# Kernel optimization log

Measured on AMD Instinct MI355X. Metric: run time of the kernel, lower is better.

## Reference

```python
import jax, jax.numpy as jnp
import numpy as np

N_HEADS = 16
LOCAL_WINDOW = 512
ROPE_BASE = 10000.0


def _rotate_half(x):
    # interleaved rotate: out[..., 2i] = -x[..., 2i+1], out[..., 2i+1] = x[..., 2i]
    x1 = x[..., 0::2]
    x2 = x[..., 1::2]
    return jnp.stack((-x2, x1), axis=-1).reshape(x.shape)


def _rope_cache(T, hd, dtype):
    half = hd // 2
    inv_freq = 1.0 / (ROPE_BASE ** (jnp.arange(half, dtype=dtype) / half))
    t = jnp.arange(T, dtype=dtype)
    freqs = t[:, None] * inv_freq[None, :]  # [T, half]
    cos = jnp.repeat(jnp.cos(freqs), 2, axis=-1)  # [T, hd]
    sin = jnp.repeat(jnp.sin(freqs), 2, axis=-1)
    return cos, sin


def setup_inputs() -> dict:
    key = jax.random.key(0)
    k1, k2, k3, k4 = jax.random.split(key, 4)
    B, T, C = 2, 2048, 1024
    x = jax.random.normal(k1, (B, T, C), dtype=jnp.float32)
    Wqkv = jax.random.normal(k2, (3 * C, C), dtype=jnp.float32) * 0.02
    Wproj = jax.random.normal(k3, (C, C), dtype=jnp.float32) * 0.02
    bproj = jax.random.normal(k4, (C,), dtype=jnp.float32) * 0.02
    return {"x": x, "Wqkv": Wqkv, "Wproj": Wproj, "bproj": bproj}


def reference(x, Wqkv, Wproj, bproj):
    B, T, C = x.shape
    H = N_HEADS
    hd = C // H
    qkv = (x @ Wqkv.T).reshape(B, T, 3, H, hd).transpose(2, 0, 3, 1, 4)  # [3,B,H,T,hd]
    q, k, v = qkv[0], qkv[1], qkv[2]
    cos, sin = _rope_cache(T, hd, x.dtype)
    cos = cos[None, None]  # [1,1,T,hd]
    sin = sin[None, None]
    q = q * cos + _rotate_half(q) * sin
    k = k * cos + _rotate_half(k) * sin
    scale = 1.0 / jnp.sqrt(jnp.asarray(hd, dtype=x.dtype))
    scores = jnp.einsum('bhqd,bhkd->bhqk', q, k) * scale  # [B,H,T,T]
    i = jnp.arange(T)[:, None]
    j = jnp.arange(T)[None, :]
    allow = (j <= i) & (jnp.abs(i - j) <= LOCAL_WINDOW)  # causal & local band
    scores = jnp.where(allow[None, None], scores, jnp.asarray(-jnp.inf, dtype=x.dtype))
    attn = jax.nn.softmax(scores, axis=-1)
    y = jnp.einsum('bhqk,bhkd->bhqd', attn, v)  # [B,H,T,hd]
    y = y.transpose(0, 2, 1, 3).reshape(B, T, C)
    return y @ Wproj.T + bproj
```

## Files before the change

### kernel.cpp

```cpp
#include <hip/hip_runtime.h>
#include <math.h>

#define B_   2
#define T_   2048
#define C_   1024
#define H_   16
#define HD_  64
#define WIN_ 512
#define BT_  (B_ * T_)

typedef __bf16 bf16x8 __attribute__((ext_vector_type(8)));
typedef float  f32x4  __attribute__((ext_vector_type(4)));
typedef unsigned int u32x2 __attribute__((ext_vector_type(2)));

__device__ __forceinline__ f32x4 mfma16(bf16x8 a, bf16x8 b, f32x4 c) {
    return __builtin_amdgcn_mfma_f32_16x16x32_bf16(a, b, c, 0, 0, 0);
}
__device__ __forceinline__ unsigned short f2b(float f) {
    __bf16 h = (__bf16)f;
    unsigned short u;
    __builtin_memcpy(&u, &h, 2);
    return u;
}
__device__ __forceinline__ void async_copy16(__bf16* lds, const __bf16* g) {
    __builtin_amdgcn_global_load_lds(
        (const __attribute__((address_space(1))) void*)g,
        (__attribute__((address_space(3))) void*)lds,
        16, 0, 0);
}

#define TR16(dst, va, OFFLIT) \
    asm volatile("ds_read_b64_tr_b16 %0, %1 offset:" OFFLIT : "=v"(dst) : "v"(va))

__device__ __forceinline__ bf16x8 combine_tr(u32x2 a, u32x2 b) {
    union { unsigned u[4]; bf16x8 v; } x;
    x.u[0] = a[0]; x.u[1] = a[1]; x.u[2] = b[0]; x.u[3] = b[1];
    return x.v;
}

__global__ void rope_table_k(float* __restrict__ cosT, float* __restrict__ sinT) {
    int gid = blockIdx.x * blockDim.x + threadIdx.x;
    if (gid >= T_ * 32) return;
    int t = gid >> 5, j = gid & 31;
    float inv = powf(10000.0f, -(float)j / 32.0f);
    float f = (float)t * inv;
    cosT[gid] = cosf(f);
    sinT[gid] = sinf(f);
}

__global__ void cvt_bf16_k(const float* __restrict__ src, __bf16* __restrict__ dst, int n8) {
    int gid = blockIdx.x * blockDim.x + threadIdx.x;
    if (gid >= n8) return;
    float4 a = *(const float4*)&src[(size_t)gid * 8];
    float4 b = *(const float4*)&src[(size_t)gid * 8 + 4];
    bf16x8 o;
    o[0] = (__bf16)a.x; o[1] = (__bf16)a.y; o[2] = (__bf16)a.z; o[3] = (__bf16)a.w;
    o[4] = (__bf16)b.x; o[5] = (__bf16)b.y; o[6] = (__bf16)b.z; o[7] = (__bf16)b.w;
    *(bf16x8*)&dst[(size_t)gid * 8] = o;
}

template<bool OUT_BF16, bool ROPE>
__global__ __launch_bounds__(256) void gemm_bt_mfma(
        const __bf16* __restrict__ A, const __bf16* __restrict__ Bm,
        const float* __restrict__ bias, void* __restrict__ Cv,
        int M, int N, int K,
        const float* __restrict__ cosT, const float* __restrict__ sinT)
{
    __shared__ __bf16 As[128 * 32];
    __shared__ __bf16 Bs[128 * 32];
    const int tid  = threadIdx.x;
    const int w    = tid >> 6;
    const int lane = tid & 63;
    const int c    = lane & 15;
    const int g    = lane >> 4;
    const int bm0  = blockIdx.y * 128;
    const int bn0  = blockIdx.x * 128;
    const int wm0  = (w >> 1) * 64;
    const int wn0  = (w & 1) * 64;

    f32x4 acc[4][4] = {};

    for (int k0 = 0; k0 < K; k0 += 32) {
        #pragma unroll
        for (int it = 0; it < 2; ++it) {
            int slot = it * 256 + tid;
            int r    = slot >> 2;
            int c8   = (slot & 3) * 8;
            async_copy16(&As[slot * 8], &A[(size_t)(bm0 + r) * K + k0 + c8]);
            async_copy16(&Bs[slot * 8], &Bm[(size_t)(bn0 + r) * K + k0 + c8]);
        }
        __syncthreads();
        bf16x8 af[4], bfr[4];
        #pragma unroll
        for (int m = 0; m < 4; ++m)
            af[m] = *(const bf16x8*)&As[(wm0 + m * 16 + c) * 32 + g * 8];
        #pragma unroll
        for (int n = 0; n < 4; ++n)
            bfr[n] = *(const bf16x8*)&Bs[(wn0 + n * 16 + c) * 32 + g * 8];
        #pragma unroll
        for (int m = 0; m < 4; ++m)
            #pragma unroll
            for (int n = 0; n < 4; ++n)
                acc[m][n] = mfma16(af[m], bfr[n], acc[m][n]);
        __syncthreads();
    }

    if (ROPE) {
        #pragma unroll
        for (int m = 0; m < 4; ++m) {
            #pragma unroll
            for (int r2 = 0; r2 < 4; ++r2) {
                const int row = bm0 + wm0 + m * 16 + g * 4 + r2;
                const int t = row & (T_ - 1);
                #pragma unroll
                for (int n = 0; n < 4; ++n) {
                    const int cbase = bn0 + wn0 + n * 16;
                    const int cc = cbase + c;
                    float v = acc[m][n][r2];
                    float outv;
                    if (cbase < 2048) {
                        float prt = __shfl_xor(v, 1);
                        int jj = (cc & 63) >> 1;
                        float cs = cosT[t * 32 + jj];
                        float sn = sinT[t * 32 + jj];
                        outv = (cc & 1) ? (v * cs + prt * sn) : (v * cs - prt * sn);
                    } else {
                        outv = v;
                    }
                    ((__bf16*)Cv)[(size_t)row * N + cc] = (__bf16)outv;
                }
            }
        }
    } else {
        #pragma unroll
        for (int m = 0; m < 4; ++m) {
            int rr = bm0 + wm0 + m * 16 + g * 4;
            #pragma unroll
            for (int n = 0; n < 4; ++n) {
                int cc = bn0 + wn0 + n * 16 + c;
                float bv = (!OUT_BF16 && bias) ? bias[cc] : 0.f;
                #pragma unroll
                for (int r2 = 0; r2 < 4; ++r2) {
                    float v = acc[m][n][r2] + bv;
                    if (OUT_BF16) ((__bf16*)Cv)[(size_t)(rr + r2) * N + cc] = (__bf16)v;
                    else          ((float*)Cv)[(size_t)(rr + r2) * N + cc] = v;
                }
            }
        }
    }
}

__global__ __launch_bounds__(256) void attn_k(const __bf16* __restrict__ qkv,
                                              __bf16* __restrict__ y)
{
    __shared__ __align__(16) unsigned short Ks[64 * 72];
    __shared__ __align__(16) unsigned short Ps[64 * 72];
    __shared__ __align__(16) unsigned short Vs[4 * 1040];

    const int tid  = threadIdx.x;
    const int lane = tid & 63;
    const int w    = tid >> 6;
    const int c    = lane & 15;
    const int g    = lane >> 4;

    const int q0 = blockIdx.x * 64;
    const int h  = blockIdx.y;
    const int b  = blockIdx.z;

    bf16x8 qa[2];
    {
        const int qrow = q0 + w * 16 + c;
        const __bf16* qp = qkv + (size_t)(b * T_ + qrow) * 3072 + h * 64 + g * 8;
        bf16x8 r0 = *(const bf16x8*)qp;
        bf16x8 r1 = *(const bf16x8*)(qp + 32);
        #pragma unroll
        for (int e = 0; e < 8; ++e) {
            qa[0][e] = (__bf16)((float)r0[e] * 0.125f);
            qa[1][e] = (__bf16)((float)r1[e] * 0.125f);
        }
    }

    float m_run[4] = {-1e30f, -1e30f, -1e30f, -1e30f};
    float l_run[4] = {0.f, 0.f, 0.f, 0.f};
    f32x4 o[4] = {};

    unsigned vs_lane;
    {
        auto* p3 = (__attribute__((address_space(3))) const unsigned short*)Vs;
        vs_lane = (unsigned)(unsigned long long)p3 + (unsigned)(g * 256 + c * 8);
    }

    const int j_start = (q0 >= WIN_) ? (q0 - WIN_) : 0;

    for (int j0 = j_start; j0 <= q0; j0 += 64) {
        __syncthreads();
        #pragma unroll
        for (int it = 0; it < 4; ++it) {
            int slot = tid + it * 256;
            int row  = slot >> 4;
            int d4   = (slot & 15) << 2;
            const __bf16* kp = qkv + (size_t)(b * T_ + j0 + row) * 3072 + 1024 + h * 64 + d4;
            *(ushort4*)&Ks[row * 72 + d4] = *(const ushort4*)kp;
            *(ushort4*)&Vs[(d4 >> 4) * 1040 + row * 16 + (d4 & 15)] = *(const ushort4*)(kp + 1024);
        }
        __syncthreads();

        f32x4 sc[4];
        #pragma unroll
        for (int nt = 0; nt < 4; ++nt) {
            const bf16x8 b0 = *(const bf16x8*)&Ks[(nt * 16 + c) * 72 + g * 8];
            const bf16x8 b1 = *(const bf16x8*)&Ks[(nt * 16 + c) * 72 + 32 + g * 8];
            f32x4 s = {0.f, 0.f, 0.f, 0.f};
            s = mfma16(qa[0], b0, s);
            s = mfma16(qa[1], b1, s);
            sc[nt] = s;
        }

        const int rlo = q0 + w * 16;
        const bool need_mask = (j0 + 63 > rlo) || (rlo + 15 - j0 > WIN_);
        if (need_mask) {
            #pragma unroll
            for (int reg = 0; reg < 4; ++reg) {
                const int i_abs = rlo + g * 4 + reg;
                #pragma unroll
                for (int nt = 0; nt < 4; ++nt) {
                    int j_abs = j0 + nt * 16 + c;
                    bool ok = (j_abs <= i_abs) && (i_abs - j_abs <= WIN_);
                    sc[nt][reg] = ok ? sc[nt][reg] : -1e30f;
                }
            }
        }

        float pmax[4];
        #pragma unroll
        for (int reg = 0; reg < 4; ++reg) {
            float bm = fmaxf(fmaxf(sc[0][reg], sc[1][reg]), fmaxf(sc[2][reg], sc[3][reg]));
            #pragma unroll
            for (int off = 1; off < 16; off <<= 1)
                bm = fmaxf(bm, __shfl_xor(bm, off));
            pmax[reg] = bm;
        }
        int need = 0;
        #pragma unroll
        for (int reg = 0; reg < 4; ++reg)
            need |= (pmax[reg] > m_run[reg] + 8.f) ? 1 : 0;
        if (__any(need)) {
            #pragma unroll
            for (int reg = 0; reg < 4; ++reg) {
                float mn = fmaxf(m_run[reg], pmax[reg]);
                float corr = __expf(m_run[reg] - mn);
                m_run[reg] = mn;
                l_run[reg] *= corr;
                #pragma unroll
                for (int dt = 0; dt < 4; ++dt) o[dt][reg] *= corr;
            }
        }
        #pragma unroll
        for (int reg = 0; reg < 4; ++reg) {
            #pragma unroll
            for (int nt = 0; nt < 4; ++nt) {
                float p = __expf(sc[nt][reg] - m_run[reg]);
                l_run[reg] += p;
                Ps[(w * 16 + g * 4 + reg) * 72 + nt * 16 + c] = f2b(p);
            }
        }

        const bf16x8 pa0 = *(const bf16x8*)&Ps[(w * 16 + c) * 72 + g * 8];
        const bf16x8 pa1 = *(const bf16x8*)&Ps[(w * 16 + c) * 72 + 32 + g * 8];
        u32x2 t0[4], t1[4], t2[4], t3[4];
        #pragma unroll
        for (int dt = 0; dt < 4; ++dt) {
            unsigned va = vs_lane + dt * 2080;
            TR16(t0[dt], va, "0");
            TR16(t1[dt], va, "128");
            TR16(t2[dt], va, "1024");
            TR16(t3[dt], va, "1152");
        }
        asm volatile("s_waitcnt lgkmcnt(0)" ::: "memory");
        __builtin_amdgcn_sched_barrier(0);
        #pragma unroll
        for (int dt = 0; dt < 4; ++dt) {
            bf16x8 vb0 = combine_tr(t0[dt], t1[dt]);
            bf16x8 vb1 = combine_tr(t2[dt], t3[dt]);
            o[dt] = mfma16(pa0, vb0, o[dt]);
            o[dt] = mfma16(pa1, vb1, o[dt]);
        }
    }

    float inv_l[4];
    #pragma unroll
    for (int reg = 0; reg < 4; ++reg) {
        float L = l_run[reg];
        #pragma unroll
        for (int off = 1; off < 16; off <<= 1)
            L += __shfl_xor(L, off);
        inv_l[reg] = 1.f / L;
    }
    #pragma unroll
    for (int dt = 0; dt < 4; ++dt)
        #pragma unroll
        for (int reg = 0; reg < 4; ++reg) {
            size_t row = (size_t)(b * T_ + q0 + w * 16 + g * 4 + reg);
            y[row * 1024 + h * 64 + dt * 16 + c] = (__bf16)(o[dt][reg] * inv_l[reg]);
        }
}

extern "C" void kernel_launch(void* const* d_in, const int* in_sizes, int n_in,
                              void* d_out, int out_size, void* d_ws, size_t ws_size,
                              hipStream_t stream) {
    const float* x     = (const float*)d_in[0];
    const float* Wqkv  = (const float*)d_in[1];
    const float* Wproj = (const float*)d_in[2];
    const float* bproj = (const float*)d_in[3];
    float* out = (float*)d_out;

    char* p = (char*)d_ws;
    float*  cosT   = (float*)p;   p += (size_t)T_ * 32 * 4;
    float*  sinT   = (float*)p;   p += (size_t)T_ * 32 * 4;
    __bf16* xb     = (__bf16*)p;  p += (size_t)BT_ * 1024 * 2;
    __bf16* Wqkvb  = (__bf16*)p;  p += (size_t)3072 * 1024 * 2;
    __bf16* Wprojb = (__bf16*)p;  p += (size_t)1024 * 1024 * 2;
    __bf16* qkvb   = (__bf16*)p;  p += (size_t)BT_ * 3072 * 2;
    __bf16* yb     = (__bf16*)p;  p += (size_t)BT_ * 1024 * 2;

    rope_table_k<<<(T_ * 32) / 256, 256, 0, stream>>>(cosT, sinT);

    cvt_bf16_k<<<(BT_ * 1024 / 8) / 256, 256, 0, stream>>>(x, xb, BT_ * 1024 / 8);
    cvt_bf16_k<<<(3072 * 1024 / 8) / 256, 256, 0, stream>>>(Wqkv, Wqkvb, 3072 * 1024 / 8);
    cvt_bf16_k<<<(1024 * 1024 / 8) / 256, 256, 0, stream>>>(Wproj, Wprojb, 1024 * 1024 / 8);

    dim3 g1(3072 / 128, BT_ / 128);
    gemm_bt_mfma<true, true><<<g1, 256, 0, stream>>>(
        xb, Wqkvb, nullptr, qkvb, BT_, 3072, 1024, cosT, sinT);

    dim3 ga(T_ / 64, H_, B_);
    attn_k<<<ga, 256, 0, stream>>>(qkvb, yb);

    dim3 g2(1024 / 128, BT_ / 128);
    gemm_bt_mfma<false, false><<<g2, 256, 0, stream>>>(
        yb, Wprojb, bproj, out, BT_, 1024, 1024, nullptr, nullptr);
}
```

Baseline: 139.3 us.

## Fuse prep kernels, double-buffer GEMM LDS, prefetch attention K/V, swizzle blocks

Merges the rope-table and three fp32-to-bf16 conversion kernels into one launch. The GEMM now double-buffers its LDS tiles so the next async load overlaps compute, with one barrier per k-step instead of two. The attention kernel prefetches the next K/V tile into registers with wider 16-byte loads, uses a 1D grid with a block swizzle to spread heads and batches across XCDs, and raises wave priority around the MFMA sections. These changes target launch overhead and exposed memory latency, at the cost of more LDS and registers, which may lower occupancy.

```diff
diff --git a/kernel.cpp b/kernel.cpp
--- a/kernel.cpp
+++ b/kernel.cpp
@@ -12,6 +12,7 @@
 typedef __bf16 bf16x8 __attribute__((ext_vector_type(8)));
 typedef float  f32x4  __attribute__((ext_vector_type(4)));
 typedef unsigned int u32x2 __attribute__((ext_vector_type(2)));
+typedef unsigned short u16x8 __attribute__((ext_vector_type(8)));
 
 __device__ __forceinline__ f32x4 mfma16(bf16x8 a, bf16x8 b, f32x4 c) {
     return __builtin_amdgcn_mfma_f32_16x16x32_bf16(a, b, c, 0, 0, 0);
@@ -38,25 +39,39 @@
     return x.v;
 }
 
-__global__ void rope_table_k(float* __restrict__ cosT, float* __restrict__ sinT) {
-    int gid = blockIdx.x * blockDim.x + threadIdx.x;
-    if (gid >= T_ * 32) return;
-    int t = gid >> 5, j = gid & 31;
-    float inv = powf(10000.0f, -(float)j / 32.0f);
-    float f = (float)t * inv;
-    cosT[gid] = cosf(f);
-    sinT[gid] = sinf(f);
-}
-
-__global__ void cvt_bf16_k(const float* __restrict__ src, __bf16* __restrict__ dst, int n8) {
-    int gid = blockIdx.x * blockDim.x + threadIdx.x;
-    if (gid >= n8) return;
-    float4 a = *(const float4*)&src[(size_t)gid * 8];
-    float4 b = *(const float4*)&src[(size_t)gid * 8 + 4];
-    bf16x8 o;
-    o[0] = (__bf16)a.x; o[1] = (__bf16)a.y; o[2] = (__bf16)a.z; o[3] = (__bf16)a.w;
-    o[4] = (__bf16)b.x; o[5] = (__bf16)b.y; o[6] = (__bf16)b.z; o[7] = (__bf16)b.w;
-    *(bf16x8*)&dst[(size_t)gid * 8] = o;
+__global__ void prep_k(const float* __restrict__ x, const float* __restrict__ Wqkv,
+                       const float* __restrict__ Wproj,
+                       __bf16* __restrict__ xb, __bf16* __restrict__ Wqkvb,
+                       __bf16* __restrict__ Wprojb,
+                       float* __restrict__ cosT, float* __restrict__ sinT) {
+    const int gid = blockIdx.x * 256 + threadIdx.x;
+    const int N0 = BT_ * 1024 / 8;
+    const int N1 = N0 + 3072 * 1024 / 8;
+    const int N2 = N1 + 1024 * 1024 / 8;
+    const int N3 = N2 + T_ * 32 / 8;
+    if (gid < N2) {
+        const float* src; __bf16* dst; int off;
+        if (gid < N0)      { src = x;     dst = xb;     off = gid; }
+        else if (gid < N1) { src = Wqkv;  dst = Wqkvb;  off = gid - N0; }
+        else               { src = Wproj; dst = Wprojb; off = gid - N1; }
+        float4 a = *(const float4*)&src[(size_t)off * 8];
+        float4 b = *(const float4*)&src[(size_t)off * 8 + 4];
+        bf16x8 o;
+        o[0] = (__bf16)a.x; o[1] = (__bf16)a.y; o[2] = (__bf16)a.z; o[3] = (__bf16)a.w;
+        o[4] = (__bf16)b.x; o[5] = (__bf16)b.y; o[6] = (__bf16)b.z; o[7] = (__bf16)b.w;
+        *(bf16x8*)&dst[(size_t)off * 8] = o;
+    } else if (gid < N3) {
+        const int r = gid - N2;
+        #pragma unroll
+        for (int e = 0; e < 8; ++e) {
+            int idx = r * 8 + e;
+            int t = idx >> 5, j = idx & 31;
+            float inv = powf(10000.0f, -(float)j / 32.0f);
+            float f = (float)t * inv;
+            cosT[idx] = cosf(f);
+            sinT[idx] = sinf(f);
+        }
+    }
 }
 
 template<bool OUT_BF16, bool ROPE>
@@ -66,8 +81,8 @@
         int M, int N, int K,
         const float* __restrict__ cosT, const float* __restrict__ sinT)
 {
-    __shared__ __bf16 As[128 * 32];
-    __shared__ __bf16 Bs[128 * 32];
+    __shared__ __bf16 As[2][128 * 32];
+    __shared__ __bf16 Bs[2][128 * 32];
     const int tid  = threadIdx.x;
     const int w    = tid >> 6;
     const int lane = tid & 63;
@@ -80,29 +95,35 @@
 
     f32x4 acc[4][4] = {};
 
-    for (int k0 = 0; k0 < K; k0 += 32) {
+    auto stage = [&](int buf, int k0) {
         #pragma unroll
         for (int it = 0; it < 2; ++it) {
             int slot = it * 256 + tid;
             int r    = slot >> 2;
             int c8   = (slot & 3) * 8;
-            async_copy16(&As[slot * 8], &A[(size_t)(bm0 + r) * K + k0 + c8]);
-            async_copy16(&Bs[slot * 8], &Bm[(size_t)(bn0 + r) * K + k0 + c8]);
-        }
+            async_copy16(&As[buf][slot * 8], &A[(size_t)(bm0 + r) * K + k0 + c8]);
+            async_copy16(&Bs[buf][slot * 8], &Bm[(size_t)(bn0 + r) * K + k0 + c8]);
+        }
+    };
+
+    stage(0, 0);
+    int cur = 0;
+    for (int k0 = 0; k0 < K; k0 += 32) {
         __syncthreads();
+        if (k0 + 32 < K) stage(cur ^ 1, k0 + 32);
         bf16x8 af[4], bfr[4];
         #pragma unroll
         for (int m = 0; m < 4; ++m)
-            af[m] = *(const bf16x8*)&As[(wm0 + m * 16 + c) * 32 + g * 8];
+            af[m] = *(const bf16x8*)&As[cur][(wm0 + m * 16 + c) * 32 + g * 8];
         #pragma unroll
         for (int n = 0; n < 4; ++n)
-            bfr[n] = *(const bf16x8*)&Bs[(wn0 + n * 16 + c) * 32 + g * 8];
+            bfr[n] = *(const bf16x8*)&Bs[cur][(wn0 + n * 16 + c) * 32 + g * 8];
         #pragma unroll
         for (int m = 0; m < 4; ++m)
             #pragma unroll
             for (int n = 0; n < 4; ++n)
                 acc[m][n] = mfma16(af[m], bfr[n], acc[m][n]);
-        __syncthreads();
+        cur ^= 1;
     }
 
     if (ROPE) {
@@ -163,9 +184,12 @@
     const int c    = lane & 15;
     const int g    = lane >> 4;
 
-    const int q0 = blockIdx.x * 64;
-    const int h  = blockIdx.y;
-    const int b  = blockIdx.z;
+    const int bid = blockIdx.x;
+    const int swz = (bid & 7) * 128 + (bid >> 3);
+    const int q0 = (swz & 31) * 64;
+    const int hb = swz >> 5;
+    const int h  = hb & 15;
+    const int b  = hb >> 4;
 
     bf16x8 qa[2];
     {
@@ -190,22 +214,44 @@
         vs_lane = (unsigned)(unsigned long long)p3 + (unsigned)(g * 256 + c * 8);
     }
 
+    const int r0s = tid >> 3,          d80 = (tid & 7) * 8;
+    const int r1s = (tid + 256) >> 3,  d81 = d80;
+    const size_t kbase = (size_t)(b * T_) * 3072 + 1024 + h * 64;
+
     const int j_start = (q0 >= WIN_) ? (q0 - WIN_) : 0;
+
+    u16x8 kr0, kr1, vr0, vr1;
+    {
+        const __bf16* p0 = qkv + kbase + (size_t)(j_start + r0s) * 3072 + d80;
+        const __bf16* p1 = qkv + kbase + (size_t)(j_start + r1s) * 3072 + d81;
+        kr0 = *(const u16x8*)p0;  vr0 = *(const u16x8*)(p0 + 1024);
+        kr1 = *(const u16x8*)p1;  vr1 = *(const u16x8*)(p1 + 1024);
+    }
 
     for (int j0 = j_start; j0 <= q0; j0 += 64) {
         __syncthreads();
-        #pragma unroll
-        for (int it = 0; it < 4; ++it) {
-            int slot = tid + it * 256;
-            int row  = slot >> 4;
-            int d4   = (slot & 15) << 2;
-            const __bf16* kp = qkv + (size_t)(b * T_ + j0 + row) * 3072 + 1024 + h * 64 + d4;
-            *(ushort4*)&Ks[row * 72 + d4] = *(const ushort4*)kp;
-            *(ushort4*)&Vs[(d4 >> 4) * 1040 + row * 16 + (d4 & 15)] = *(const ushort4*)(kp + 1024);
+        {
+            union { u16x8 v; ushort4 h[2]; } u;
+            u.v = kr0;
+            *(ushort4*)&Ks[r0s * 72 + d80]     = u.h[0];
+            *(ushort4*)&Ks[r0s * 72 + d80 + 4] = u.h[1];
+            u.v = kr1;
+            *(ushort4*)&Ks[r1s * 72 + d81]     = u.h[0];
+            *(ushort4*)&Ks[r1s * 72 + d81 + 4] = u.h[1];
+            *(u16x8*)&Vs[(d80 >> 4) * 1040 + r0s * 16 + (d80 & 15)] = vr0;
+            *(u16x8*)&Vs[(d81 >> 4) * 1040 + r1s * 16 + (d81 & 15)] = vr1;
         }
         __syncthreads();
 
+        if (j0 + 64 <= q0) {
+            const __bf16* p0 = qkv + kbase + (size_t)(j0 + 64 + r0s) * 3072 + d80;
+            const __bf16* p1 = qkv + kbase + (size_t)(j0 + 64 + r1s) * 3072 + d81;
+            kr0 = *(const u16x8*)p0;  vr0 = *(const u16x8*)(p0 + 1024);
+            kr1 = *(const u16x8*)p1;  vr1 = *(const u16x8*)(p1 + 1024);
+        }
+
         f32x4 sc[4];
+        __builtin_amdgcn_s_setprio(1);
         #pragma unroll
         for (int nt = 0; nt < 4; ++nt) {
             const bf16x8 b0 = *(const bf16x8*)&Ks[(nt * 16 + c) * 72 + g * 8];
@@ -215,6 +261,7 @@
             s = mfma16(qa[1], b1, s);
             sc[nt] = s;
         }
+        __builtin_amdgcn_s_setprio(0);
 
         const int rlo = q0 + w * 16;
         const bool need_mask = (j0 + 63 > rlo) || (rlo + 15 - j0 > WIN_);
@@ -278,6 +325,7 @@
         }
         asm volatile("s_waitcnt lgkmcnt(0)" ::: "memory");
         __builtin_amdgcn_sched_barrier(0);
+        __builtin_amdgcn_s_setprio(1);
         #pragma unroll
         for (int dt = 0; dt < 4; ++dt) {
             bf16x8 vb0 = combine_tr(t0[dt], t1[dt]);
@@ -285,6 +333,7 @@
             o[dt] = mfma16(pa0, vb0, o[dt]);
             o[dt] = mfma16(pa1, vb1, o[dt]);
         }
+        __builtin_amdgcn_s_setprio(0);
     }
 
     float inv_l[4];
@@ -323,18 +372,15 @@
     __bf16* qkvb   = (__bf16*)p;  p += (size_t)BT_ * 3072 * 2;
     __bf16* yb     = (__bf16*)p;  p += (size_t)BT_ * 1024 * 2;
 
-    rope_table_k<<<(T_ * 32) / 256, 256, 0, stream>>>(cosT, sinT);
-
-    cvt_bf16_k<<<(BT_ * 1024 / 8) / 256, 256, 0, stream>>>(x, xb, BT_ * 1024 / 8);
-    cvt_bf16_k<<<(3072 * 1024 / 8) / 256, 256, 0, stream>>>(Wqkv, Wqkvb, 3072 * 1024 / 8);
-    cvt_bf16_k<<<(1024 * 1024 / 8) / 256, 256, 0, stream>>>(Wproj, Wprojb, 1024 * 1024 / 8);
+    const int nprep = (BT_ * 1024 + 3072 * 1024 + 1024 * 1024) / 8 + T_ * 32 / 8;
+    prep_k<<<(nprep + 255) / 256, 256, 0, stream>>>(
+        x, Wqkv, Wproj, xb, Wqkvb, Wprojb, cosT, sinT);
 
     dim3 g1(3072 / 128, BT_ / 128);
     gemm_bt_mfma<true, true><<<g1, 256, 0, stream>>>(
         xb, Wqkvb, nullptr, qkvb, BT_, 3072, 1024, cosT, sinT);
 
-    dim3 ga(T_ / 64, H_, B_);
-    attn_k<<<ga, 256, 0, stream>>>(qkvb, yb);
+    attn_k<<<(T_ / 64) * H_ * B_, 256, 0, stream>>>(qkvb, yb);
 
     dim3 g2(1024 / 128, BT_ / 128);
     gemm_bt_mfma<false, false><<<g2, 256, 0, stream>>>(
```

Result: faster. 125.7 us (-9.8%).
